# Optimization experiments

Measured on AMD Instinct MI355X. Metric: run time of the kernel, lower is better.

## Reference

```python
import jax, jax.numpy as jnp
import numpy as np

EMBED_DIM = 1024
ATTEN_DIM = 64


def setup_inputs() -> dict:
    key = jax.random.key(0)
    k_x, k_q, k_k, k_v = jax.random.split(key, 4)
    B, S = 4, 4096
    scale = 1.0 / np.sqrt(EMBED_DIM)
    x = jax.random.normal(k_x, (B, S, EMBED_DIM), dtype=jnp.float32)
    # torch nn.Linear weights are [out_features, in_features]
    Wq = jax.random.normal(k_q, (ATTEN_DIM, EMBED_DIM), dtype=jnp.float32) * scale
    Wk = jax.random.normal(k_k, (ATTEN_DIM, EMBED_DIM), dtype=jnp.float32) * scale
    Wv = jax.random.normal(k_v, (ATTEN_DIM, EMBED_DIM), dtype=jnp.float32) * scale
    return {"x": x, "Wq": Wq, "Wk": Wk, "Wv": Wv}


def reference(x, Wq, Wk, Wv):
    # q, k, v: [B, S, D]
    q = jnp.einsum('bse,de->bsd', x, Wq)
    k = jnp.einsum('bse,de->bsd', x, Wk)
    v = jnp.einsum('bse,de->bsd', x, Wv)
    d = k.shape[-1]
    scores = jnp.einsum('bsd,btd->bst', q, k) / jnp.sqrt(jnp.float32(d))
    S = x.shape[1]
    causal = jnp.tril(jnp.ones((S, S), dtype=bool))
    scores = jnp.where(causal[None, :, :], scores, -jnp.inf)
    attn = jax.nn.softmax(scores, axis=-1)
    return jnp.einsum('bst,btd->bsd', attn, v)
```

## Files before the change

### kernel.cpp

```cpp
#include <hip/hip_runtime.h>
#include <hip/hip_bf16.h>
#include <stdint.h>

typedef __attribute__((ext_vector_type(8))) short  short8;
typedef __attribute__((ext_vector_type(4))) short  short4v;
typedef __attribute__((ext_vector_type(4))) float  float4v;
typedef __attribute__((ext_vector_type(16))) float f32x16;
typedef __attribute__((ext_vector_type(2))) unsigned int uint2v;

#define MFMA16(a, b, c) __builtin_amdgcn_mfma_f32_16x16x32_bf16((a), (b), (c), 0, 0, 0)
#define MFMA32(a, b, c) __builtin_amdgcn_mfma_f32_32x32x16_bf16((a), (b), (c), 0, 0, 0)

#define S_LEN  4096
#define NBATCH 4
#define EMB    1024
#define DD     64
#define NROWS  (NBATCH * S_LEN)
#define SCL2   0.1803368801111204f

#define AS1 const __attribute__((address_space(1))) unsigned int*
#define AS3 __attribute__((address_space(3))) unsigned int*

static __device__ __forceinline__ short f2bf(float f) {
  uint32_t u = __float_as_uint(f);
  return (short)((u + 0x7FFFu + ((u >> 16) & 1u)) >> 16);
}
static __device__ __forceinline__ unsigned pk2(float a, float b) {
  union { __hip_bfloat162 h; unsigned u; } z;
  z.h = __float22bfloat162_rn(make_float2(a, b));
  return z.u;
}
static __device__ __forceinline__ short8 cvt8(float4v a, float4v b) {
  union { unsigned u[4]; short8 s; } z;
  z.u[0] = pk2(a[0], a[1]); z.u[1] = pk2(a[2], a[3]);
  z.u[2] = pk2(b[0], b[1]); z.u[3] = pk2(b[2], b[3]);
  return z.s;
}

__global__ void wcvt_kernel(const float* __restrict__ Wq, const float* __restrict__ Wk,
                            const float* __restrict__ Wv, short* __restrict__ Wb2) {
  const int t   = blockIdx.x * 256 + threadIdx.x;
  const int row = t >> 7;
  const int k   = (t & 127) * 8;
  const float* src = (row < 64) ? (Wq + (size_t)row * EMB)
                   : (row < 128) ? (Wk + (size_t)(row - 64) * EMB)
                                 : (Wv + (size_t)(row - 128) * EMB);
  const float sc = (row < 64) ? SCL2 : 1.0f;
  float4v a = *(const float4v*)(src + k);
  float4v b = *(const float4v*)(src + k + 4);
#pragma unroll
  for (int i = 0; i < 4; ++i) { a[i] *= sc; b[i] *= sc; }
  *(short8*)(Wb2 + (((k >> 5) * 192 + row) << 5) + (k & 31)) = cvt8(a, b);
}

__global__ __launch_bounds__(256, 2) void qkv_kernel(
    const float* __restrict__ x, const short* __restrict__ Wb2,
    short* __restrict__ Qb, short* __restrict__ Kb, short* __restrict__ Vt) {
  __shared__ float As[2][2048];
  __shared__ short Bs[2][12288];

  const int tid  = threadIdx.x;
  const int w    = tid >> 6;
  const int lane = tid & 63;
  const int ln   = lane & 15;
  const int quad = lane >> 4;
  const int m0   = blockIdx.x * 32;
  const int wr   = w & 1;
  const int wc   = w >> 1;

  const int tA0 = 2 * w, tA1 = 2 * w + 1;
  const float* xA0 = x + (size_t)(m0 + ((tA0 >> 2) << 4) + (lane >> 2)) * EMB
                       + ((tA0 & 3) * 4 + (lane & 3)) * 4;
  const float* xA1 = x + (size_t)(m0 + ((tA1 >> 2) << 4) + (lane >> 2)) * EMB
                       + ((tA1 & 3) * 4 + (lane & 3)) * 4;
  const short* wB = Wb2 + (size_t)(6 * w) * 512 + lane * 8;

#define STAGE(S, BUF) do {                                                      \
    __builtin_amdgcn_global_load_lds((AS1)(xA0 + (S) * 64),                     \
        (AS3)&As[BUF][tA0 * 256], 16, 0, 0);                                    \
    __builtin_amdgcn_global_load_lds((AS1)(xA1 + (S) * 64),                     \
        (AS3)&As[BUF][tA1 * 256], 16, 0, 0);                                    \
    _Pragma("unroll")                                                           \
    for (int j = 0; j < 6; ++j)                                                 \
      __builtin_amdgcn_global_load_lds((AS1)(wB + (size_t)(S) * 12288 + j * 512),\
          (AS3)&Bs[BUF][(6 * w + j) * 512], 16, 0, 0);                          \
  } while (0)

  const float4v zz = {0.f, 0.f, 0.f, 0.f};
  float4v acc[6] = {zz, zz, zz, zz, zz, zz};

  STAGE(0, 0);
  int buf = 0;
  for (int s = 0; s < 16; ++s) {
    __syncthreads();
    if (s + 1 < 16) STAGE(s + 1, buf ^ 1);
    short8 aF[2];
#pragma unroll
    for (int h = 0; h < 2; ++h) {
      const int ai = (wr * 4 + 2 * h + (quad >> 1)) * 256 + (ln * 4 + (quad & 1) * 2) * 4;
      const float4v lo = *(const float4v*)&As[buf][ai];
      const float4v hi = *(const float4v*)&As[buf][ai + 4];
      aF[h] = cvt8(lo, hi);
    }
#pragma unroll
    for (int f = 0; f < 6; ++f) {
      const int cf = wc * 6 + f;
      const short8 b0 = *(const short8*)&Bs[buf][(cf * 16 + ln) * 32 + quad * 8];
      const short8 b1 = *(const short8*)&Bs[buf][6144 + (cf * 16 + ln) * 32 + quad * 8];
      if (wc == 0 || f < 2) {
        acc[f] = MFMA16(aF[0], b0, acc[f]);
        acc[f] = MFMA16(aF[1], b1, acc[f]);
      } else {
        acc[f] = MFMA16(b0, aF[0], acc[f]);
        acc[f] = MFMA16(b1, aF[1], acc[f]);
      }
    }
    buf ^= 1;
  }
#undef STAGE

  const int b  = m0 >> 12;
  const int sb = m0 & (S_LEN - 1);
  if (wc == 0) {
#pragma unroll
    for (int f = 0; f < 6; ++f)
#pragma unroll
      for (int r = 0; r < 4; ++r) {
        const int row = m0 + wr * 16 + quad * 4 + r;
        if (f < 4) Qb[(size_t)row * DD + f * 16 + ln] = f2bf(acc[f][r]);
        else       Kb[(size_t)row * DD + (f - 4) * 16 + ln] = f2bf(acc[f][r]);
      }
  } else {
#pragma unroll
    for (int f = 0; f < 2; ++f)
#pragma unroll
      for (int r = 0; r < 4; ++r) {
        const int row = m0 + wr * 16 + quad * 4 + r;
        Kb[(size_t)row * DD + 32 + f * 16 + ln] = f2bf(acc[f][r]);
      }
#pragma unroll
    for (int f = 2; f < 6; ++f)
#pragma unroll
      for (int r = 0; r < 4; ++r) {
        const int d = (f - 2) * 16 + quad * 4 + r;
        Vt[((size_t)b * DD + d) * S_LEN + sb + wr * 16 + ln] = f2bf(acc[f][r]);
      }
  }
}

__global__ __launch_bounds__(512, 4) void attn_kernel(
    const short* __restrict__ Qb, const short* __restrict__ Kb,
    const short* __restrict__ Vt, float* __restrict__ out) {
  __shared__ float sbuf[8][2048];
  __shared__ float llds[8][32];

  const int tid  = threadIdx.x;
  const int w    = tid >> 6;
  const int lane = tid & 63;
  const int l31  = lane & 31;
  const int hi   = lane >> 5;
  const int g    = blockIdx.x;
  const int u    = g & 255;
  const int half = g >> 8;
  const int b    = u & 3;
  const int jj   = u >> 2;
  const int band = half ? (127 - jj) : jj;
  const short* Kbase = Kb + (size_t)b * S_LEN * DD;
  const short* Vbase = Vt + (size_t)b * DD * S_LEN;

  const int qb    = band * 32;
  const int qg0   = b * S_LEN + qb;
  const int qglob = qb + l31;

  short8 q8[4];
#pragma unroll
  for (int dk = 0; dk < 4; ++dk)
    q8[dk] = *(const short8*)(Qb + (size_t)(qg0 + l31) * DD + dk * 16 + hi * 8);

  f32x16 o0, o1;
  f32x16 zz16;
#pragma unroll
  for (int e = 0; e < 16; ++e) { o0[e] = 0.f; o1[e] = 0.f; zz16[e] = 0.f; }
  float lp = 0.f;

  const int T32 = band + 1;

  for (int it = w; it < T32; it += 8) {
    const int kv0 = it * 32;
    short8 kf[4];
#pragma unroll
    for (int dk = 0; dk < 4; ++dk)
      kf[dk] = *(const short8*)(Kbase + (size_t)(kv0 + l31) * DD + dk * 16 + hi * 8);
    short8 vf[2][2];
#pragma unroll
    for (int df = 0; df < 2; ++df)
#pragma unroll
      for (int kc = 0; kc < 2; ++kc)
        vf[df][kc] = *(const short8*)(Vbase + (size_t)(df * 32 + l31) * S_LEN + kv0 + kc * 16 + hi * 8);

    f32x16 s = MFMA32(kf[0], q8[0], zz16);
#pragma unroll
    for (int dk = 1; dk < 4; ++dk)
      s = MFMA32(kf[dk], q8[dk], s);

    if (it == band) {
#pragma unroll
      for (int e = 0; e < 16; ++e) {
        const int kvl = (e & 3) + 8 * (e >> 2) + 4 * hi;
        float e0 = __builtin_amdgcn_exp2f(fminf(s[e], 60.0f));
        if (kv0 + kvl > qglob) e0 = 0.f;
        s[e] = e0;
        lp += e0;
      }
    } else {
#pragma unroll
      for (int e = 0; e < 16; ++e) {
        float e0 = __builtin_amdgcn_exp2f(fminf(s[e], 60.0f));
        s[e] = e0;
        lp += e0;
      }
    }

    {
      unsigned ua, ub, uc, ud, ue, uf2, ug, uh;
      asm("v_cvt_pk_bf16_f32 %0, %1, %2" : "=v"(ua) : "v"(s[0]),  "v"(s[1]));
      asm("v_cvt_pk_bf16_f32 %0, %1, %2" : "=v"(ub) : "v"(s[2]),  "v"(s[3]));
      asm("v_cvt_pk_bf16_f32 %0, %1, %2" : "=v"(uc) : "v"(s[4]),  "v"(s[5]));
      asm("v_cvt_pk_bf16_f32 %0, %1, %2" : "=v"(ud) : "v"(s[6]),  "v"(s[7]));
      asm("v_cvt_pk_bf16_f32 %0, %1, %2" : "=v"(ue) : "v"(s[8]),  "v"(s[9]));
      asm("v_cvt_pk_bf16_f32 %0, %1, %2" : "=v"(uf2): "v"(s[10]), "v"(s[11]));
      asm("v_cvt_pk_bf16_f32 %0, %1, %2" : "=v"(ug) : "v"(s[12]), "v"(s[13]));
      asm("v_cvt_pk_bf16_f32 %0, %1, %2" : "=v"(uh) : "v"(s[14]), "v"(s[15]));
      uint2v r0 = __builtin_amdgcn_permlane32_swap(ua, uc, false, false);
      uint2v r1 = __builtin_amdgcn_permlane32_swap(ub, ud, false, false);
      uint2v r2 = __builtin_amdgcn_permlane32_swap(ue, ug, false, false);
      uint2v r3 = __builtin_amdgcn_permlane32_swap(uf2, uh, false, false);
      union { unsigned uu[4]; short8 s8; } p0, p1;
      p0.uu[0] = r0[0]; p0.uu[1] = r1[0]; p0.uu[2] = r0[1]; p0.uu[3] = r1[1];
      p1.uu[0] = r2[0]; p1.uu[1] = r3[0]; p1.uu[2] = r2[1]; p1.uu[3] = r3[1];
      o0 = MFMA32(p0.s8, vf[0][0], o0);
      o0 = MFMA32(p1.s8, vf[0][1], o0);
      o1 = MFMA32(p0.s8, vf[1][0], o1);
      o1 = MFMA32(p1.s8, vf[1][1], o1);
    }
  }

  lp += __shfl_xor(lp, 32);
  float* pw = &sbuf[w][0];
#pragma unroll
  for (int e = 0; e < 16; ++e) {
    const int ql = (e & 3) + 8 * (e >> 2) + 4 * hi;
    pw[ql * 64 + l31]      = o0[e];
    pw[ql * 64 + 32 + l31] = o1[e];
  }
  if (hi == 0) llds[w][l31] = lp;
  __syncthreads();

#pragma unroll
  for (int jx = 0; jx < 4; ++jx) {
    const int idx = tid + jx * 512;
    const int row = idx >> 6, col = idx & 63;
    float sum = 0.f, lt = 0.f;
#pragma unroll
    for (int wi = 0; wi < 8; ++wi) {
      sum += sbuf[wi][row * 64 + col];
      lt  += llds[wi][row];
    }
    out[(size_t)(qg0 + row) * DD + col] = sum * __builtin_amdgcn_rcpf(lt);
  }
}

extern "C" void kernel_launch(void* const* d_in, const int* in_sizes, int n_in,
                              void* d_out, int out_size, void* d_ws, size_t ws_size,
                              hipStream_t stream) {
  const float* x  = (const float*)d_in[0];
  const float* Wq = (const float*)d_in[1];
  const float* Wk = (const float*)d_in[2];
  const float* Wv = (const float*)d_in[3];

  short* Qb  = (short*)d_ws;
  short* Kb  = Qb + (size_t)NROWS * DD;
  short* Vt  = Kb + (size_t)NROWS * DD;
  short* Wb2 = Vt + (size_t)NROWS * DD;

  wcvt_kernel<<<dim3(96), dim3(256), 0, stream>>>(Wq, Wk, Wv, Wb2);
  qkv_kernel<<<dim3(NROWS / 32), dim3(256), 0, stream>>>(x, Wb2, Qb, Kb, Vt);
  attn_kernel<<<dim3(NBATCH * 128), dim3(512), 0, stream>>>(Qb, Kb, Vt, (float*)d_out);
}
```

Before: 153.9 us.

## Split long causal bands across two blocks and merge partials in a combine kernel

The attention grid grows from 512 to 768 blocks: the 64 longest query bands per batch have their KV range split in half across two blocks, and the rest run whole. Each block writes unnormalized partial outputs and row sums to workspace, and a new combine kernel adds the partials and normalizes. This targets load imbalance and tail effects from the causal triangle. In exchange it adds a launch and extra global traffic for the partials.

```diff
diff --git a/kernel.cpp b/kernel.cpp
--- a/kernel.cpp
+++ b/kernel.cpp
@@ -150,7 +150,7 @@
 
 __global__ __launch_bounds__(512, 4) void attn_kernel(
     const short* __restrict__ Qb, const short* __restrict__ Kb,
-    const short* __restrict__ Vt, float* __restrict__ out) {
+    const short* __restrict__ Vt, float* __restrict__ Op, float* __restrict__ Lp) {
   __shared__ float sbuf[8][2048];
   __shared__ float llds[8][32];
 
@@ -160,11 +160,18 @@
   const int l31  = lane & 31;
   const int hi   = lane >> 5;
   const int g    = blockIdx.x;
-  const int u    = g & 255;
-  const int half = g >> 8;
-  const int b    = u & 3;
-  const int jj   = u >> 2;
-  const int band = half ? (127 - jj) : jj;
+  const int b    = g & 3;
+  const int r    = g >> 2;
+  int band, it0, itN;
+  if (r < 128) {
+    band = 127 - (r >> 1);
+    const int h = (band + 1) >> 1;
+    if (r & 1) { it0 = h; itN = band + 1; }
+    else       { it0 = 0; itN = h; }
+  } else {
+    band = 191 - r;
+    it0 = 0; itN = band + 1;
+  }
   const short* Kbase = Kb + (size_t)b * S_LEN * DD;
   const short* Vbase = Vt + (size_t)b * DD * S_LEN;
 
@@ -183,9 +190,7 @@
   for (int e = 0; e < 16; ++e) { o0[e] = 0.f; o1[e] = 0.f; zz16[e] = 0.f; }
   float lp = 0.f;
 
-  const int T32 = band + 1;
-
-  for (int it = w; it < T32; it += 8) {
+  for (int it = it0 + w; it < itN; it += 8) {
     const int kv0 = it * 32;
     short8 kf[4];
 #pragma unroll
@@ -266,7 +271,37 @@
       sum += sbuf[wi][row * 64 + col];
       lt  += llds[wi][row];
     }
-    out[(size_t)(qg0 + row) * DD + col] = sum * __builtin_amdgcn_rcpf(lt);
+    Op[(size_t)g * 2048 + idx] = sum;
+    if (col == 0) Lp[g * 32 + row] = lt;
+  }
+}
+
+__global__ __launch_bounds__(256) void comb_kernel(
+    const float* __restrict__ Op, const float* __restrict__ Lp,
+    float* __restrict__ out) {
+  const int cb    = blockIdx.x;
+  const int batch = cb & 3;
+  const int j     = cb >> 2;
+  int gA, gB = -1;
+  if (j >= 64) { const int r0 = 2 * (127 - j); gA = (r0 << 2) | batch; gB = gA + 4; }
+  else         { gA = ((191 - j) << 2) | batch; }
+
+  __shared__ float ls[32];
+  if (threadIdx.x < 32) {
+    float l = Lp[gA * 32 + threadIdx.x];
+    if (gB >= 0) l += Lp[gB * 32 + threadIdx.x];
+    ls[threadIdx.x] = __builtin_amdgcn_rcpf(l);
+  }
+  __syncthreads();
+
+  const size_t rowg0 = (size_t)batch * S_LEN + (size_t)j * 32;
+#pragma unroll
+  for (int jx = 0; jx < 8; ++jx) {
+    const int idx = threadIdx.x + jx * 256;
+    const int row = idx >> 6, col = idx & 63;
+    float v = Op[(size_t)gA * 2048 + idx];
+    if (gB >= 0) v += Op[(size_t)gB * 2048 + idx];
+    out[(rowg0 + row) * DD + col] = v * ls[row];
   }
 }
 
@@ -282,8 +317,11 @@
   short* Kb  = Qb + (size_t)NROWS * DD;
   short* Vt  = Kb + (size_t)NROWS * DD;
   short* Wb2 = Vt + (size_t)NROWS * DD;
+  float* Op  = (float*)((char*)d_ws + (8u << 20));
+  float* Lp  = Op + (size_t)768 * 2048;
 
   wcvt_kernel<<<dim3(96), dim3(256), 0, stream>>>(Wq, Wk, Wv, Wb2);
   qkv_kernel<<<dim3(NROWS / 32), dim3(256), 0, stream>>>(x, Wb2, Qb, Kb, Vt);
-  attn_kernel<<<dim3(NBATCH * 128), dim3(512), 0, stream>>>(Qb, Kb, Vt, (float*)d_out);
-}
+  attn_kernel<<<dim3(768), dim3(512), 0, stream>>>(Qb, Kb, Vt, Op, Lp);
+  comb_kernel<<<dim3(512), dim3(256), 0, stream>>>(Op, Lp, (float*)d_out);
+}
```

Result: slower. 163.8 us (+6.4%).

## Process two adjacent query bands per block to share K/V tile loads

Applied to the files above, without the earlier changes.

Each attention block now computes two consecutive 32-row query bands, reusing every loaded K and V tile for both bands, and the grid is halved. Launch bounds are lowered to allow more registers for the doubled accumulators. This removes the previous mirrored band pairing across blocks, so per-block work becomes strongly imbalanced along the causal triangle and the longest block does roughly twice the compute on its critical path.

```diff
diff --git a/kernel.cpp b/kernel.cpp
--- a/kernel.cpp
+++ b/kernel.cpp
@@ -148,7 +148,7 @@
   }
 }
 
-__global__ __launch_bounds__(512, 4) void attn_kernel(
+__global__ __launch_bounds__(512, 2) void attn_kernel(
     const short* __restrict__ Qb, const short* __restrict__ Kb,
     const short* __restrict__ Vt, float* __restrict__ out) {
   __shared__ float sbuf[8][2048];
@@ -160,32 +160,32 @@
   const int l31  = lane & 31;
   const int hi   = lane >> 5;
   const int g    = blockIdx.x;
-  const int u    = g & 255;
-  const int half = g >> 8;
-  const int b    = u & 3;
-  const int jj   = u >> 2;
-  const int band = half ? (127 - jj) : jj;
+  const int b    = g & 3;
+  const int k2   = g >> 2;
   const short* Kbase = Kb + (size_t)b * S_LEN * DD;
   const short* Vbase = Vt + (size_t)b * DD * S_LEN;
 
-  const int qb    = band * 32;
-  const int qg0   = b * S_LEN + qb;
-  const int qglob = qb + l31;
-
-  short8 q8[4];
-#pragma unroll
-  for (int dk = 0; dk < 4; ++dk)
-    q8[dk] = *(const short8*)(Qb + (size_t)(qg0 + l31) * DD + dk * 16 + hi * 8);
-
-  f32x16 o0, o1;
-  f32x16 zz16;
-#pragma unroll
-  for (int e = 0; e < 16; ++e) { o0[e] = 0.f; o1[e] = 0.f; zz16[e] = 0.f; }
-  float lp = 0.f;
-
-  const int T32 = band + 1;
-
-  for (int it = w; it < T32; it += 8) {
+  const int bandA = 2 * k2, bandB = 2 * k2 + 1;
+  const int qbA   = bandA * 32;
+  const int qgA   = b * S_LEN + qbA;
+  const int qglobA = qbA + l31;
+  const int qglobB = qbA + 32 + l31;
+
+  short8 qA[4], qB[4];
+#pragma unroll
+  for (int dk = 0; dk < 4; ++dk) {
+    qA[dk] = *(const short8*)(Qb + (size_t)(qgA + l31) * DD + dk * 16 + hi * 8);
+    qB[dk] = *(const short8*)(Qb + (size_t)(qgA + 32 + l31) * DD + dk * 16 + hi * 8);
+  }
+
+  f32x16 oA0, oA1, oB0, oB1, zz16;
+#pragma unroll
+  for (int e = 0; e < 16; ++e) { oA0[e] = oA1[e] = oB0[e] = oB1[e] = 0.f; zz16[e] = 0.f; }
+  float lpA = 0.f, lpB = 0.f;
+
+  const int itN = bandB + 1;
+
+  for (int it = w; it < itN; it += 8) {
     const int kv0 = it * 32;
     short8 kf[4];
 #pragma unroll
@@ -198,76 +198,83 @@
       for (int kc = 0; kc < 2; ++kc)
         vf[df][kc] = *(const short8*)(Vbase + (size_t)(df * 32 + l31) * S_LEN + kv0 + kc * 16 + hi * 8);
 
-    f32x16 s = MFMA32(kf[0], q8[0], zz16);
-#pragma unroll
-    for (int dk = 1; dk < 4; ++dk)
-      s = MFMA32(kf[dk], q8[dk], s);
-
-    if (it == band) {
-#pragma unroll
-      for (int e = 0; e < 16; ++e) {
-        const int kvl = (e & 3) + 8 * (e >> 2) + 4 * hi;
-        float e0 = __builtin_amdgcn_exp2f(fminf(s[e], 60.0f));
-        if (kv0 + kvl > qglob) e0 = 0.f;
-        s[e] = e0;
-        lp += e0;
-      }
-    } else {
-#pragma unroll
-      for (int e = 0; e < 16; ++e) {
-        float e0 = __builtin_amdgcn_exp2f(fminf(s[e], 60.0f));
-        s[e] = e0;
-        lp += e0;
-      }
-    }
-
-    {
-      unsigned ua, ub, uc, ud, ue, uf2, ug, uh;
-      asm("v_cvt_pk_bf16_f32 %0, %1, %2" : "=v"(ua) : "v"(s[0]),  "v"(s[1]));
-      asm("v_cvt_pk_bf16_f32 %0, %1, %2" : "=v"(ub) : "v"(s[2]),  "v"(s[3]));
-      asm("v_cvt_pk_bf16_f32 %0, %1, %2" : "=v"(uc) : "v"(s[4]),  "v"(s[5]));
-      asm("v_cvt_pk_bf16_f32 %0, %1, %2" : "=v"(ud) : "v"(s[6]),  "v"(s[7]));
-      asm("v_cvt_pk_bf16_f32 %0, %1, %2" : "=v"(ue) : "v"(s[8]),  "v"(s[9]));
-      asm("v_cvt_pk_bf16_f32 %0, %1, %2" : "=v"(uf2): "v"(s[10]), "v"(s[11]));
-      asm("v_cvt_pk_bf16_f32 %0, %1, %2" : "=v"(ug) : "v"(s[12]), "v"(s[13]));
-      asm("v_cvt_pk_bf16_f32 %0, %1, %2" : "=v"(uh) : "v"(s[14]), "v"(s[15]));
-      uint2v r0 = __builtin_amdgcn_permlane32_swap(ua, uc, false, false);
-      uint2v r1 = __builtin_amdgcn_permlane32_swap(ub, ud, false, false);
-      uint2v r2 = __builtin_amdgcn_permlane32_swap(ue, ug, false, false);
-      uint2v r3 = __builtin_amdgcn_permlane32_swap(uf2, uh, false, false);
-      union { unsigned uu[4]; short8 s8; } p0, p1;
-      p0.uu[0] = r0[0]; p0.uu[1] = r1[0]; p0.uu[2] = r0[1]; p0.uu[3] = r1[1];
-      p1.uu[0] = r2[0]; p1.uu[1] = r3[0]; p1.uu[2] = r2[1]; p1.uu[3] = r3[1];
-      o0 = MFMA32(p0.s8, vf[0][0], o0);
-      o0 = MFMA32(p1.s8, vf[0][1], o0);
-      o1 = MFMA32(p0.s8, vf[1][0], o1);
-      o1 = MFMA32(p1.s8, vf[1][1], o1);
-    }
-  }
-
-  lp += __shfl_xor(lp, 32);
-  float* pw = &sbuf[w][0];
-#pragma unroll
-  for (int e = 0; e < 16; ++e) {
-    const int ql = (e & 3) + 8 * (e >> 2) + 4 * hi;
-    pw[ql * 64 + l31]      = o0[e];
-    pw[ql * 64 + 32 + l31] = o1[e];
-  }
-  if (hi == 0) llds[w][l31] = lp;
-  __syncthreads();
-
-#pragma unroll
-  for (int jx = 0; jx < 4; ++jx) {
-    const int idx = tid + jx * 512;
-    const int row = idx >> 6, col = idx & 63;
-    float sum = 0.f, lt = 0.f;
-#pragma unroll
-    for (int wi = 0; wi < 8; ++wi) {
-      sum += sbuf[wi][row * 64 + col];
-      lt  += llds[wi][row];
-    }
-    out[(size_t)(qg0 + row) * DD + col] = sum * __builtin_amdgcn_rcpf(lt);
-  }
+#define BAND_STEP(QV, OV0, OV1, LP, QGLOB, DIAG, SKIP) do {                    \
+    if (!(SKIP)) {                                                             \
+      f32x16 s = MFMA32(kf[0], (QV)[0], zz16);                                 \
+      _Pragma("unroll")                                                        \
+      for (int dk = 1; dk < 4; ++dk) s = MFMA32(kf[dk], (QV)[dk], s);          \
+      if (DIAG) {                                                              \
+        _Pragma("unroll")                                                      \
+        for (int e = 0; e < 16; ++e) {                                         \
+          const int kvl = (e & 3) + 8 * (e >> 2) + 4 * hi;                     \
+          float e0 = __builtin_amdgcn_exp2f(fminf(s[e], 60.0f));               \
+          if (kv0 + kvl > (QGLOB)) e0 = 0.f;                                   \
+          s[e] = e0; (LP) += e0;                                               \
+        }                                                                      \
+      } else {                                                                 \
+        _Pragma("unroll")                                                      \
+        for (int e = 0; e < 16; ++e) {                                         \
+          float e0 = __builtin_amdgcn_exp2f(fminf(s[e], 60.0f));               \
+          s[e] = e0; (LP) += e0;                                               \
+        }                                                                      \
+      }                                                                        \
+      unsigned ua, ub, uc, ud, ue, uf2, ug, uh;                                \
+      asm("v_cvt_pk_bf16_f32 %0, %1, %2" : "=v"(ua) : "v"(s[0]),  "v"(s[1]));  \
+      asm("v_cvt_pk_bf16_f32 %0, %1, %2" : "=v"(ub) : "v"(s[2]),  "v"(s[3]));  \
+      asm("v_cvt_pk_bf16_f32 %0, %1, %2" : "=v"(uc) : "v"(s[4]),  "v"(s[5]));  \
+      asm("v_cvt_pk_bf16_f32 %0, %1, %2" : "=v"(ud) : "v"(s[6]),  "v"(s[7]));  \
+      asm("v_cvt_pk_bf16_f32 %0, %1, %2" : "=v"(ue) : "v"(s[8]),  "v"(s[9]));  \
+      asm("v_cvt_pk_bf16_f32 %0, %1, %2" : "=v"(uf2): "v"(s[10]), "v"(s[11])); \
+      asm("v_cvt_pk_bf16_f32 %0, %1, %2" : "=v"(ug) : "v"(s[12]), "v"(s[13])); \
+      asm("v_cvt_pk_bf16_f32 %0, %1, %2" : "=v"(uh) : "v"(s[14]), "v"(s[15])); \
+      uint2v r0 = __builtin_amdgcn_permlane32_swap(ua, uc, false, false);      \
+      uint2v r1 = __builtin_amdgcn_permlane32_swap(ub, ud, false, false);      \
+      uint2v r2 = __builtin_amdgcn_permlane32_swap(ue, ug, false, false);      \
+      uint2v r3 = __builtin_amdgcn_permlane32_swap(uf2, uh, false, false);     \
+      union { unsigned uu[4]; short8 s8; } p0, p1;                             \
+      p0.uu[0] = r0[0]; p0.uu[1] = r1[0]; p0.uu[2] = r0[1]; p0.uu[3] = r1[1];  \
+      p1.uu[0] = r2[0]; p1.uu[1] = r3[0]; p1.uu[2] = r2[1]; p1.uu[3] = r3[1];  \
+      (OV0) = MFMA32(p0.s8, vf[0][0], (OV0));                                  \
+      (OV0) = MFMA32(p1.s8, vf[0][1], (OV0));                                  \
+      (OV1) = MFMA32(p0.s8, vf[1][0], (OV1));                                  \
+      (OV1) = MFMA32(p1.s8, vf[1][1], (OV1));                                  \
+    }                                                                          \
+  } while (0)
+
+    BAND_STEP(qA, oA0, oA1, lpA, qglobA, it == bandA, it > bandA);
+    BAND_STEP(qB, oB0, oB1, lpB, qglobB, it == bandB, false);
+#undef BAND_STEP
+  }
+
+#define EPILOG(OV0, OV1, LP, ROW0) do {                                        \
+    float lpt = (LP) + __shfl_xor((LP), 32);                                   \
+    float* pw = &sbuf[w][0];                                                   \
+    _Pragma("unroll")                                                          \
+    for (int e = 0; e < 16; ++e) {                                             \
+      const int ql = (e & 3) + 8 * (e >> 2) + 4 * hi;                          \
+      pw[ql * 64 + l31]      = (OV0)[e];                                       \
+      pw[ql * 64 + 32 + l31] = (OV1)[e];                                       \
+    }                                                                          \
+    if (hi == 0) llds[w][l31] = lpt;                                           \
+    __syncthreads();                                                           \
+    _Pragma("unroll")                                                          \
+    for (int jx = 0; jx < 4; ++jx) {                                           \
+      const int idx = tid + jx * 512;                                          \
+      const int row = idx >> 6, col = idx & 63;                                \
+      float sum = 0.f, lt = 0.f;                                               \
+      _Pragma("unroll")                                                        \
+      for (int wi = 0; wi < 8; ++wi) {                                         \
+        sum += sbuf[wi][row * 64 + col];                                       \
+        lt  += llds[wi][row];                                                  \
+      }                                                                        \
+      out[(size_t)((ROW0) + row) * DD + col] = sum * __builtin_amdgcn_rcpf(lt);\
+    }                                                                          \
+    __syncthreads();                                                           \
+  } while (0)
+
+  EPILOG(oA0, oA1, lpA, qgA);
+  EPILOG(oB0, oB1, lpB, qgA + 32);
+#undef EPILOG
 }
 
 extern "C" void kernel_launch(void* const* d_in, const int* in_sizes, int n_in,
@@ -285,5 +292,5 @@
 
   wcvt_kernel<<<dim3(96), dim3(256), 0, stream>>>(Wq, Wk, Wv, Wb2);
   qkv_kernel<<<dim3(NROWS / 32), dim3(256), 0, stream>>>(x, Wb2, Qb, Kb, Vt);
-  attn_kernel<<<dim3(NBATCH * 128), dim3(512), 0, stream>>>(Qb, Kb, Vt, (float*)d_out);
-}
+  attn_kernel<<<dim3(NBATCH * 64), dim3(512), 0, stream>>>(Qb, Kb, Vt, (float*)d_out);
+}
```

After: 154.3 us. No clear change (+0.3%).
